# Kernel tuning notes

Hardware: AMD Instinct MI355X
Metric: run time of the kernel (lower is better)

The kernel has to match this reference:

```python
import jax, jax.numpy as jnp
import numpy as np

B, C, IC, H, W = 2, 64, 32, 96, 96


def setup_inputs() -> dict:
    key = jax.random.key(0)
    ks = jax.random.split(key, 8)
    s_in = 1.0 / np.sqrt(C)
    s_ic = 1.0 / np.sqrt(IC)
    return {
        "x": jax.random.normal(ks[0], (B, C, H, W), dtype=jnp.float32),
        "Wg": jax.random.uniform(ks[1], (IC, C), jnp.float32, -s_in, s_in),
        "bg": jax.random.uniform(ks[2], (IC,), jnp.float32, -s_in, s_in),
        "Wt": jax.random.uniform(ks[3], (IC, C), jnp.float32, -s_in, s_in),
        "bt": jax.random.uniform(ks[4], (IC,), jnp.float32, -s_in, s_in),
        "Wp": jax.random.uniform(ks[5], (IC, C), jnp.float32, -s_in, s_in),
        "bp": jax.random.uniform(ks[6], (IC,), jnp.float32, -s_in, s_in),
        "Wo": jax.random.uniform(ks[7], (C, IC), jnp.float32, -s_ic, s_ic),
        "bo": jax.random.uniform(jax.random.fold_in(key, 9), (C,), jnp.float32, -s_ic, s_ic),
    }


def reference(x, Wg, bg, Wt, bt, Wp, bp, Wo, bo):
    b, c, h, w = x.shape
    n = h * w
    xf = x.reshape(b, c, n)  # [B, C, N]

    def proj(Wc, bc):  # 1x1 conv == channel GEMM -> [B, IC, N]
        return jnp.einsum("bcn,oc->bon", xf, Wc) + bc[None, :, None]

    g = proj(Wg, bg)
    theta = proj(Wt, bt)
    phi = proj(Wp, bp)
    scores = jnp.einsum("bcn,bcm->bnm", theta, phi)  # [B, N, N]
    att = jax.nn.softmax(scores, axis=-1)
    y = jnp.einsum("bnm,bcm->bcn", att, g)  # [B, IC, N]
    o = jnp.einsum("bcn,oc->bon", y, Wo) + bo[None, :, None]  # [B, C, N]
    return o.reshape(b, c, h, w) + x
```

## Files before the change

### kernel.cpp

```cpp
#include <hip/hip_runtime.h>
#include <hip/hip_bf16.h>


#define B_   2
#define C_   64
#define IC_  32
#define N_   9216
#define LOG2E 1.44269504088896f

typedef __attribute__((ext_vector_type(4))) float  f32x4;
typedef __attribute__((ext_vector_type(8))) short  s16x8;
typedef __attribute__((ext_vector_type(4))) short  s16x4;

static __device__ __forceinline__ ushort f2bf(float f) {
  union { __hip_bfloat16 h; ushort u; } cv;
  cv.h = __float2bfloat16(f);
  return cv.u;
}

static __device__ __forceinline__ float bf2f(ushort u) {
  union { uint i; float f; } c;
  c.i = ((uint)u) << 16;
  return c.f;
}

static __device__ __forceinline__ f32x4 mfma32(s16x8 a, s16x8 b, f32x4 c) {
  return __builtin_amdgcn_mfma_f32_16x16x32_bf16(a, b, c, 0, 0, 0);
}

__global__ __launch_bounds__(256) void proj_kernel(
    const float* __restrict__ x,
    const float* __restrict__ Wg, const float* __restrict__ bg,
    const float* __restrict__ Wt, const float* __restrict__ bt,
    const float* __restrict__ Wp, const float* __restrict__ bp,
    ushort* __restrict__ Qb, ushort* __restrict__ Kb, ushort* __restrict__ Vt)
{
  const int grp = blockIdx.x / 72;
  const int ic0 = grp * 8;
  const int bn  = (blockIdx.x % 72) * 256 + threadIdx.x;
  const int b   = bn / N_;
  const int n   = bn % N_;

  float ag[8], at_[8], ap[8];
#pragma unroll
  for (int j = 0; j < 8; ++j) { ag[j] = 0.f; at_[j] = 0.f; ap[j] = 0.f; }

  const float* xp = x + (size_t)b * C_ * N_ + n;
#pragma unroll 8
  for (int c = 0; c < C_; ++c) {
    const float xv = xp[(size_t)c * N_];
#pragma unroll
    for (int j = 0; j < 8; ++j) {
      ag[j]  = fmaf(Wg[(ic0 + j) * C_ + c], xv, ag[j]);
      at_[j] = fmaf(Wt[(ic0 + j) * C_ + c], xv, at_[j]);
      ap[j]  = fmaf(Wp[(ic0 + j) * C_ + c], xv, ap[j]);
    }
  }

  union { ushort u[8]; s16x8 v; } qv, kv;
#pragma unroll
  for (int j = 0; j < 8; ++j) {
    const int ic = ic0 + j;
    qv.u[j] = f2bf(LOG2E * (at_[j] + bt[ic]));
    kv.u[j] = f2bf(ap[j] + bp[ic]);
  }
  *reinterpret_cast<s16x8*>(Qb + (size_t)bn * IC_ + ic0) = qv.v;
  *reinterpret_cast<s16x8*>(Kb + (size_t)bn * IC_ + ic0) = kv.v;

  const int j6 = n & 63, u = j6 >> 5, r = j6 & 31;
  const int nperm = (n - j6) + u * 32 + (r & 15) * 2 + (r >> 4);
#pragma unroll
  for (int j = 0; j < 8; ++j) {
    const int ic = ic0 + j;
    Vt[(size_t)(b * IC_ + ic) * N_ + nperm] = f2bf(ag[j] + bg[ic]);
  }
}

template<int NSEG>
__global__ __launch_bounds__(256, 4) void attn_kernel(
    const ushort* __restrict__ Qb, const ushort* __restrict__ Kb,
    const ushort* __restrict__ Vt, ushort* __restrict__ Opart,
    float* __restrict__ Lp)
{
  constexpr int NT = 144 / NSEG;
  constexpr int SKEYS = N_ / NSEG;
  constexpr int QBLK = N_ / 256;
  constexpr int KSTR = 36;
  constexpr int VSTR = 70;
  __shared__ __align__(16) ushort Kl[64 * KSTR];
  __shared__ __align__(16) ushort Vl[32 * VSTR];

  const int qblk = blockIdx.x % QBLK;
  const int bs   = blockIdx.x / QBLK;
  const int seg  = bs % NSEG;
  const int b    = bs / NSEG;
  const int key0 = seg * SKEYS;

  const int tid  = threadIdx.x;
  const int lane = tid & 63;
  const int wave = tid >> 6;
  const int q16  = lane & 15;
  const int h    = lane >> 4;

  const int qbase = qblk * 256 + wave * 64;

  const short ONE = (short)0x3F80;
  const s16x8 ones = {ONE, ONE, ONE, ONE, ONE, ONE, ONE, ONE};

  const ushort* qptr = Qb + (size_t)(b * N_ + qbase + q16) * IC_ + h * 8;
  const s16x8 qfA = *reinterpret_cast<const s16x8*>(qptr);
  const s16x8 qfB = *reinterpret_cast<const s16x8*>(qptr + 16 * IC_);
  const s16x8 qfC = *reinterpret_cast<const s16x8*>(qptr + 32 * IC_);
  const s16x8 qfD = *reinterpret_cast<const s16x8*>(qptr + 48 * IC_);

  f32x4 aA0 = {0.f,0.f,0.f,0.f}, aA1 = {0.f,0.f,0.f,0.f}, aLA = {0.f,0.f,0.f,0.f};
  f32x4 aB0 = {0.f,0.f,0.f,0.f}, aB1 = {0.f,0.f,0.f,0.f}, aLB = {0.f,0.f,0.f,0.f};
  f32x4 aC0 = {0.f,0.f,0.f,0.f}, aC1 = {0.f,0.f,0.f,0.f}, aLC = {0.f,0.f,0.f,0.f};
  f32x4 aD0 = {0.f,0.f,0.f,0.f}, aD1 = {0.f,0.f,0.f,0.f}, aLD = {0.f,0.f,0.f,0.f};

  const int krow = tid >> 2, kpart = tid & 3;
  const ushort* kg = Kb + ((size_t)b * N_ + key0 + krow) * IC_ + kpart * 8;
  ushort* kl_dst = &Kl[krow * KSTR + kpart * 8];

  const int vd = tid >> 3, vpp = tid & 7;
  const ushort* vg = Vt + (size_t)(b * IC_ + vd) * N_ + key0 + vpp * 8;
  ushort* vl_dst = &Vl[vd * VSTR + vpp * 8];

  s16x8 kreg = *reinterpret_cast<const s16x8*>(kg);
  s16x8 vreg = *reinterpret_cast<const s16x8*>(vg);

  for (int it = 0; it < NT; ++it) {
    *reinterpret_cast<s16x8*>(kl_dst) = kreg;
    *reinterpret_cast<s16x8*>(vl_dst) = vreg;
    __syncthreads();

    if (it + 1 < NT) {
      kg += 64 * IC_;
      vg += 64;
      kreg = *reinterpret_cast<const s16x8*>(kg);
      vreg = *reinterpret_cast<const s16x8*>(vg);
    }

#pragma unroll
    for (int u = 0; u < 2; ++u) {
      const s16x8 kf0 = *reinterpret_cast<const s16x8*>(&Kl[(u * 32 + q16) * KSTR + h * 8]);
      const s16x8 kf1 = *reinterpret_cast<const s16x8*>(&Kl[(u * 32 + 16 + q16) * KSTR + h * 8]);
      const s16x8 vf0 = *reinterpret_cast<const s16x8*>(&Vl[q16 * VSTR + u * 32 + h * 8]);
      const s16x8 vf1 = *reinterpret_cast<const s16x8*>(&Vl[(16 + q16) * VSTR + u * 32 + h * 8]);
      const f32x4 z = {0.f, 0.f, 0.f, 0.f};

#define DO_FRAG(QF, A0, A1, AL)                                              \
      {                                                                      \
        __builtin_amdgcn_s_setprio(1);                                       \
        const f32x4 s0 = mfma32(kf0, QF, z);                                 \
        const f32x4 s1 = mfma32(kf1, QF, z);                                 \
        __builtin_amdgcn_s_setprio(0);                                       \
        union { __hip_bfloat162 h2[4]; s16x8 v; } pa;                        \
        _Pragma("unroll")                                                    \
        for (int i = 0; i < 4; ++i) {                                        \
          float2 f2;                                                         \
          f2.x = __builtin_amdgcn_exp2f(s0[i]);                              \
          f2.y = __builtin_amdgcn_exp2f(s1[i]);                              \
          pa.h2[i] = __float22bfloat162_rn(f2);                              \
        }                                                                    \
        __builtin_amdgcn_s_setprio(1);                                       \
        A0 = mfma32(pa.v, vf0, A0);                                          \
        A1 = mfma32(pa.v, vf1, A1);                                          \
        AL = mfma32(pa.v, ones, AL);                                         \
        __builtin_amdgcn_s_setprio(0);                                       \
      }

      DO_FRAG(qfA, aA0, aA1, aLA)
      DO_FRAG(qfB, aB0, aB1, aLB)
      DO_FRAG(qfC, aC0, aC1, aLC)
      DO_FRAG(qfD, aD0, aD1, aLD)
#undef DO_FRAG
    }
    __syncthreads();
  }

  const size_t obase0 = ((size_t)(b * NSEG + seg) * N_);
#pragma unroll
  for (int r = 0; r < 4; ++r) {
    const int qA = qbase + h * 4 + r;
    Opart[(obase0 + qA) * IC_ + q16]           = f2bf(aA0[r]);
    Opart[(obase0 + qA) * IC_ + 16 + q16]      = f2bf(aA1[r]);
    Opart[(obase0 + qA + 16) * IC_ + q16]      = f2bf(aB0[r]);
    Opart[(obase0 + qA + 16) * IC_ + 16 + q16] = f2bf(aB1[r]);
    Opart[(obase0 + qA + 32) * IC_ + q16]      = f2bf(aC0[r]);
    Opart[(obase0 + qA + 32) * IC_ + 16 + q16] = f2bf(aC1[r]);
    Opart[(obase0 + qA + 48) * IC_ + q16]      = f2bf(aD0[r]);
    Opart[(obase0 + qA + 48) * IC_ + 16 + q16] = f2bf(aD1[r]);
  }
  if (q16 == 0) {
#pragma unroll
    for (int r = 0; r < 4; ++r) {
      Lp[obase0 + qbase + h * 4 + r]      = aLA[r];
      Lp[obase0 + qbase + 16 + h * 4 + r] = aLB[r];
      Lp[obase0 + qbase + 32 + h * 4 + r] = aLC[r];
      Lp[obase0 + qbase + 48 + h * 4 + r] = aLD[r];
    }
  }
}

template<int NSEG>
__global__ __launch_bounds__(256) void epilogue_kernel(
    const ushort* __restrict__ Opart, const float* __restrict__ Lp,
    const float* __restrict__ Wo, const float* __restrict__ bo,
    const float* __restrict__ x, float* __restrict__ out)
{
  __shared__ float ylds[32][33];

  const int tid = threadIdx.x;
  const int bn0 = blockIdx.x * 32;

  {
    const int p  = tid >> 3;
    const int e  = tid & 7;
    const int bn = bn0 + p;
    const int b  = bn / N_;
    const int q  = bn % N_;

    float l = 0.f;
    float o[4] = {0.f, 0.f, 0.f, 0.f};
#pragma unroll
    for (int s = 0; s < NSEG; ++s) {
      const size_t base = (size_t)(b * NSEG + s) * N_ + q;
      l += Lp[base];
      union { s16x4 v; ushort us[4]; } ov;
      ov.v = *reinterpret_cast<const s16x4*>(Opart + base * IC_ + e * 4);
#pragma unroll
      for (int j = 0; j < 4; ++j) o[j] += bf2f(ov.us[j]);
    }
    const float inv = 1.0f / l;
#pragma unroll
    for (int j = 0; j < 4; ++j) ylds[p][e * 4 + j] = o[j] * inv;
  }
  __syncthreads();

  {
    const int pe  = tid & 31;
    const int g   = tid >> 5;
    const int oc0 = g * 8;
    const int bn  = bn0 + pe;
    const int b   = bn / N_;
    const int n   = bn % N_;

    float acc[8];
#pragma unroll
    for (int j = 0; j < 8; ++j) acc[j] = bo[oc0 + j];

#pragma unroll
    for (int ic = 0; ic < IC_; ++ic) {
      const float yv = ylds[pe][ic];
#pragma unroll
      for (int j = 0; j < 8; ++j)
        acc[j] = fmaf(Wo[(oc0 + j) * IC_ + ic], yv, acc[j]);
    }

#pragma unroll
    for (int j = 0; j < 8; ++j) {
      const int oc = oc0 + j;
      const size_t xi = (size_t)(b * C_ + oc) * N_ + n;
      out[xi] = acc[j] + x[xi];
    }
  }
}

extern "C" void kernel_launch(void* const* d_in, const int* in_sizes, int n_in,
                              void* d_out, int out_size, void* d_ws, size_t ws_size,
                              hipStream_t stream)
{
  const float* x  = (const float*)d_in[0];
  const float* Wg = (const float*)d_in[1];
  const float* bg = (const float*)d_in[2];
  const float* Wt = (const float*)d_in[3];
  const float* bt = (const float*)d_in[4];
  const float* Wp = (const float*)d_in[5];
  const float* bp = (const float*)d_in[6];
  const float* Wo = (const float*)d_in[7];
  const float* bo = (const float*)d_in[8];
  float* out = (float*)d_out;

  char* ws = (char*)d_ws;
  const size_t szb = (size_t)B_ * N_ * IC_ * sizeof(ushort);
  ushort* Qb = (ushort*)(ws);
  ushort* Kb = (ushort*)(ws + szb);
  ushort* Vt = (ushort*)(ws + 2 * szb);
  ushort* Op = (ushort*)(ws + 3 * szb);

  const size_t need24 = 3 * szb + 24 * szb + (size_t)24 * B_ * N_ * sizeof(float);
  const size_t need16 = 3 * szb + 16 * szb + (size_t)16 * B_ * N_ * sizeof(float);
  const int epiblocks = (B_ * N_) / 32;

  proj_kernel<<<288, 256, 0, stream>>>(x, Wg, bg, Wt, bt, Wp, bp, Qb, Kb, Vt);
  if (ws_size >= need24) {
    float* Lp = (float*)(ws + 3 * szb + 24 * szb);
    attn_kernel<24><<<B_ * 24 * (N_ / 256), 256, 0, stream>>>(Qb, Kb, Vt, Op, Lp);
    epilogue_kernel<24><<<epiblocks, 256, 0, stream>>>(Op, Lp, Wo, bo, x, out);
  } else if (ws_size >= need16) {
    float* Lp = (float*)(ws + 3 * szb + 16 * szb);
    attn_kernel<16><<<B_ * 16 * (N_ / 256), 256, 0, stream>>>(Qb, Kb, Vt, Op, Lp);
    epilogue_kernel<16><<<epiblocks, 256, 0, stream>>>(Op, Lp, Wo, bo, x, out);
  } else {
    float* Lp = (float*)(ws + 3 * szb + 8 * szb);
    attn_kernel<8><<<B_ * 8 * (N_ / 256), 256, 0, stream>>>(Qb, Kb, Vt, Op, Lp);
    epilogue_kernel<8><<<epiblocks, 256, 0, stream>>>(Op, Lp, Wo, bo, x, out);
  }
}
```

Baseline: 71.48 us.

## Double-buffer K/V LDS tiles in attention kernel with two-ahead register prefetch

Splits the shared-memory K and V tiles into two buffers. Each iteration stores the next tile into the idle buffer while computing on the current one, and the register prefetch now runs two tiles ahead. This removes the barrier that used to sit between the store and the compute, so global-load latency and LDS stores overlap with the MFMA work. In exchange it doubles LDS use, which could lower occupancy, and it adds a full unroll of the tile loop that may bloat code and raise register pressure.

```diff
diff --git a/kernel.cpp b/kernel.cpp
--- a/kernel.cpp
+++ b/kernel.cpp
@@ -87,8 +87,8 @@
   constexpr int QBLK = N_ / 256;
   constexpr int KSTR = 36;
   constexpr int VSTR = 70;
-  __shared__ __align__(16) ushort Kl[64 * KSTR];
-  __shared__ __align__(16) ushort Vl[32 * VSTR];
+  __shared__ __align__(16) ushort Kl[2][64 * KSTR];
+  __shared__ __align__(16) ushort Vl[2][32 * VSTR];
 
   const int qblk = blockIdx.x % QBLK;
   const int bs   = blockIdx.x / QBLK;
@@ -120,33 +120,41 @@
 
   const int krow = tid >> 2, kpart = tid & 3;
   const ushort* kg = Kb + ((size_t)b * N_ + key0 + krow) * IC_ + kpart * 8;
-  ushort* kl_dst = &Kl[krow * KSTR + kpart * 8];
+  const int kloff = krow * KSTR + kpart * 8;
 
   const int vd = tid >> 3, vpp = tid & 7;
   const ushort* vg = Vt + (size_t)(b * IC_ + vd) * N_ + key0 + vpp * 8;
-  ushort* vl_dst = &Vl[vd * VSTR + vpp * 8];
+  const int vloff = vd * VSTR + vpp * 8;
 
   s16x8 kreg = *reinterpret_cast<const s16x8*>(kg);
   s16x8 vreg = *reinterpret_cast<const s16x8*>(vg);
-
+  *reinterpret_cast<s16x8*>(&Kl[0][kloff]) = kreg;
+  *reinterpret_cast<s16x8*>(&Vl[0][vloff]) = vreg;
+  if (NT > 1) {
+    kreg = *reinterpret_cast<const s16x8*>(kg + (size_t)64 * IC_);
+    vreg = *reinterpret_cast<const s16x8*>(vg + 64);
+  }
+  __syncthreads();
+
+#pragma unroll
   for (int it = 0; it < NT; ++it) {
-    *reinterpret_cast<s16x8*>(kl_dst) = kreg;
-    *reinterpret_cast<s16x8*>(vl_dst) = vreg;
-    __syncthreads();
-
     if (it + 1 < NT) {
-      kg += 64 * IC_;
-      vg += 64;
-      kreg = *reinterpret_cast<const s16x8*>(kg);
-      vreg = *reinterpret_cast<const s16x8*>(vg);
-    }
-
+      *reinterpret_cast<s16x8*>(&Kl[(it + 1) & 1][kloff]) = kreg;
+      *reinterpret_cast<s16x8*>(&Vl[(it + 1) & 1][vloff]) = vreg;
+    }
+    if (it + 2 < NT) {
+      kreg = *reinterpret_cast<const s16x8*>(kg + (size_t)(it + 2) * 64 * IC_);
+      vreg = *reinterpret_cast<const s16x8*>(vg + (it + 2) * 64);
+    }
+
+    const ushort* Klc = Kl[it & 1];
+    const ushort* Vlc = Vl[it & 1];
 #pragma unroll
     for (int u = 0; u < 2; ++u) {
-      const s16x8 kf0 = *reinterpret_cast<const s16x8*>(&Kl[(u * 32 + q16) * KSTR + h * 8]);
-      const s16x8 kf1 = *reinterpret_cast<const s16x8*>(&Kl[(u * 32 + 16 + q16) * KSTR + h * 8]);
-      const s16x8 vf0 = *reinterpret_cast<const s16x8*>(&Vl[q16 * VSTR + u * 32 + h * 8]);
-      const s16x8 vf1 = *reinterpret_cast<const s16x8*>(&Vl[(16 + q16) * VSTR + u * 32 + h * 8]);
+      const s16x8 kf0 = *reinterpret_cast<const s16x8*>(&Klc[(u * 32 + q16) * KSTR + h * 8]);
+      const s16x8 kf1 = *reinterpret_cast<const s16x8*>(&Klc[(u * 32 + 16 + q16) * KSTR + h * 8]);
+      const s16x8 vf0 = *reinterpret_cast<const s16x8*>(&Vlc[q16 * VSTR + u * 32 + h * 8]);
+      const s16x8 vf1 = *reinterpret_cast<const s16x8*>(&Vlc[(16 + q16) * VSTR + u * 32 + h * 8]);
       const f32x4 z = {0.f, 0.f, 0.f, 0.f};
 
 #define DO_FRAG(QF, A0, A1, AL)                                              \
```

Measured after the change: 86.72 us. +21.3%, slower.
